# Kernel tuning notes

Measured on AMD Instinct MI355X. Metric: run time of the kernel, lower is better.

Reference implementation:

```python
import jax, jax.numpy as jnp
import numpy as np

B, T, D, H = 2, 2048, 1024, 16
Dh = D // H


def _rope(q, k):
    # q, k: (B, H, T, Dh), interleaved even/odd rotation
    t = q.shape[2]
    dh = q.shape[3]
    inv_freq = 1.0 / (10000.0 ** (jnp.arange(0, dh, 2, dtype=jnp.float32) / dh))
    pos = jnp.arange(t, dtype=jnp.float32)
    freqs = pos[:, None] * inv_freq[None, :]          # (T, Dh/2)
    sin = jnp.sin(freqs)[None, None]                  # (1,1,T,Dh/2)
    cos = jnp.cos(freqs)[None, None]

    def rot(x):
        xe, xo = x[..., ::2], x[..., 1::2]
        re = xe * cos - xo * sin
        ro = xe * sin + xo * cos
        return jnp.stack([re, ro], axis=-1).reshape(x.shape)

    return rot(q), rot(k)


def setup_inputs() -> dict:
    key = jax.random.key(0)
    k1, k2, k3 = jax.random.split(key, 3)
    s = 1.0 / np.sqrt(D)
    return {
        "x": jax.random.normal(k1, (B, T, D), dtype=jnp.float32),
        "w_qkv": jax.random.normal(k2, (3 * D, D), dtype=jnp.float32) * s,
        "b_qkv": jnp.zeros((3 * D,), dtype=jnp.float32),
        "w_out": jax.random.normal(k3, (D, D), dtype=jnp.float32) * s,
        "b_out": jnp.zeros((D,), dtype=jnp.float32),
    }


def reference(x, w_qkv, b_qkv, w_out, b_out):
    b, t, d = x.shape
    qkv = x @ w_qkv.T + b_qkv                         # (B,T,3D)
    q, k, v = jnp.split(qkv, 3, axis=-1)
    q = q.reshape(b, t, H, Dh).transpose(0, 2, 1, 3)  # (B,H,T,Dh)
    k = k.reshape(b, t, H, Dh).transpose(0, 2, 1, 3)
    v = v.reshape(b, t, H, Dh).transpose(0, 2, 1, 3)
    q, k = _rope(q, k)
    scores = jnp.einsum("bhtd,bhsd->bhts", q, k) / jnp.sqrt(jnp.float32(Dh))
    causal = jnp.tril(jnp.ones((t, t), dtype=bool))[None, None]
    scores = jnp.where(causal, scores, -jnp.inf)
    probs = jax.nn.softmax(scores, axis=-1)
    out = jnp.einsum("bhts,bhsd->bhtd", probs, v)     # (B,H,T,Dh)
    out = out.transpose(0, 2, 1, 3).reshape(b, t, d)
    return out @ w_out.T + b_out
```

## Files before the change

kernel.cpp:

```cpp
#include <hip/hip_runtime.h>
#include <hip/hip_bf16.h>
#include <math.h>
#include <type_traits>

#define B_ 2
#define T_ 2048
#define D_ 1024
#define H_ 16
#define DH_ 64

typedef __bf16 bf16_t;
typedef bf16_t bf16x8 __attribute__((ext_vector_type(8)));
typedef bf16_t bf16x4 __attribute__((ext_vector_type(4)));
typedef float f32x4 __attribute__((ext_vector_type(4)));

typedef __attribute__((address_space(1))) const void gas_void;
typedef __attribute__((address_space(3))) void las_void;

__device__ __forceinline__ void gld16(const void* g, void* l) {
    __builtin_amdgcn_global_load_lds((gas_void*)g, (las_void*)l, 16, 0, 0);
}

__global__ __launch_bounds__(256) void cvt3(const float* __restrict__ a,
                                            const float* __restrict__ b,
                                            const float* __restrict__ c,
                                            bf16_t* __restrict__ oa,
                                            bf16_t* __restrict__ ob,
                                            bf16_t* __restrict__ oc) {
    int i = blockIdx.x * 256 + threadIdx.x;
    const float* src; bf16_t* dst; int off;
    if (i < 1048576)      { src = a; dst = oa; off = i; }
    else if (i < 1835008) { src = b; dst = ob; off = i - 1048576; }
    else                  { src = c; dst = oc; off = i - 1835008; }
    float4 f = ((const float4*)src)[off];
    bf16x4 v = { (bf16_t)f.x, (bf16_t)f.y, (bf16_t)f.z, (bf16_t)f.w };
    ((bf16x4*)dst)[off] = v;
}

__global__ __launch_bounds__(256) void rope_tab_k(float2* __restrict__ tab) {
    int i = blockIdx.x * 256 + threadIdx.x;
    int t = i >> 5, d2 = i & 31;
    float invf = exp2f(-(float)d2 * 0.4152410118609203f);
    float ang = (float)t * invf;
    float sn, cs;
    sincosf(ang, &sn, &cs);
    tab[i] = make_float2(cs, sn);
}

template<int EPI>
__global__ __launch_bounds__(256) void gemm128(const bf16_t* __restrict__ A,
                                               const bf16_t* __restrict__ Bw,
                                               const float* __restrict__ bias,
                                               const float2* __restrict__ tab,
                                               bf16_t* __restrict__ q_out,
                                               bf16_t* __restrict__ k_out,
                                               bf16_t* __restrict__ vt_out,
                                               float* __restrict__ f_out,
                                               int K, int N) {
    __shared__ __align__(16) char smem[49152];
    char* b0 = smem;
    char* b1 = smem + 16384;
    char* b2 = smem + 32768;

    int tid = threadIdx.x;
    int lane = tid & 63, wid = tid >> 6;
    int wr = wid >> 1, wc = wid & 1;
    int lr = lane & 15, lk = lane >> 4;

    int l = blockIdx.y * gridDim.x + blockIdx.x;
    int chunk = (gridDim.x * gridDim.y) >> 3;
    int u = (l & 7) * chunk + (l >> 3);
    int bx = u % gridDim.x;
    int by = u / gridDim.x;

    f32x4 acc[4][4];
    f32x4 z = {0.f, 0.f, 0.f, 0.f};
#pragma unroll
    for (int i = 0; i < 4; i++)
#pragma unroll
        for (int j = 0; j < 4; j++) acc[i][j] = z;

    const char* Ab = (const char*)(A + (size_t)by * 128 * K);
    const char* Bb = (const char*)(Bw + (size_t)bx * 128 * K);
    const int rowstride = K * 2;

    int p0 = tid * 16;
    int p1 = 4096 + tid * 16;
    int r0 = p0 >> 6, r1 = p1 >> 6;
    int cb0 = (p0 & 63) ^ (((r0 >> 1) & 3) << 4);
    int cb1 = (p1 & 63) ^ (((r1 >> 1) & 3) << 4);
    size_t gA0 = (size_t)r0 * rowstride + cb0;
    size_t gA1 = (size_t)r1 * rowstride + cb1;

    int oa[4], ob[4];
#pragma unroll
    for (int m = 0; m < 4; m++) {
        int row = wr * 64 + m * 16 + lr;
        oa[m] = row * 64 + ((lk * 16) ^ (((row >> 1) & 3) << 4));
    }
#pragma unroll
    for (int n = 0; n < 4; n++) {
        int row = wc * 64 + n * 16 + lr;
        ob[n] = row * 64 + ((lk * 16) ^ (((row >> 1) & 3) << 4));
    }

    auto stg = [&](char* buf, int ks) __attribute__((always_inline)) {
        const char* Ag = Ab + (size_t)ks * 64;
        const char* Bg = Bb + (size_t)ks * 64;
        gld16(Ag + gA0, buf + p0);
        gld16(Ag + gA1, buf + p1);
        gld16(Bg + gA0, buf + 8192 + p0);
        gld16(Bg + gA1, buf + 8192 + p1);
    };

    auto iterf = [&](auto vmc, char* buf, int ks, bool dostage) __attribute__((always_inline)) {
        constexpr int VM = decltype(vmc)::value;
        if constexpr (VM == 8)      asm volatile("s_waitcnt vmcnt(8)" ::: "memory");
        else if constexpr (VM == 4) asm volatile("s_waitcnt vmcnt(4)" ::: "memory");
        else                        asm volatile("s_waitcnt vmcnt(0)" ::: "memory");
        __builtin_amdgcn_s_barrier();
        asm volatile("" ::: "memory");
        bf16x8 Af[4], Bf[4];
#pragma unroll
        for (int m = 0; m < 4; m++) Af[m] = *(const bf16x8*)(buf + oa[m]);
#pragma unroll
        for (int n = 0; n < 4; n++) Bf[n] = *(const bf16x8*)(buf + 8192 + ob[n]);
#pragma unroll
        for (int m = 0; m < 4; m++)
#pragma unroll
            for (int n = 0; n < 4; n++)
                acc[m][n] = __builtin_amdgcn_mfma_f32_16x16x32_bf16(Af[m], Bf[n], acc[m][n], 0, 0, 0);
        asm volatile("" ::: "memory");
        __builtin_amdgcn_s_barrier();
        asm volatile("" ::: "memory");
        if (dostage) stg(buf, ks);
    };

    std::integral_constant<int, 8> c8;
    std::integral_constant<int, 4> c4;
    std::integral_constant<int, 0> c0;

    stg(b0, 0);
    stg(b1, 1);
    stg(b2, 2);
    for (int s = 0; s < 30; s += 3) {
        iterf(c8, b0, s + 3, s + 3 < 32);
        iterf(c8, b1, s + 4, s + 4 < 32);
        iterf(c8, b2, s + 5, s + 5 < 32);
    }
    iterf(c4, b0, 0, false);
    iterf(c0, b1, 0, false);

    int m_base = by * 128 + wr * 64;
    int n_base = bx * 128 + wc * 64;
    if (EPI == 1) {
#pragma unroll
        for (int m = 0; m < 4; m++) {
            int gm0 = m_base + m * 16 + lk * 4;
#pragma unroll
            for (int n = 0; n < 4; n++) {
                int nc = n_base + n * 16 + lr;
                float bv = bias[nc];
#pragma unroll
                for (int j = 0; j < 4; j++)
                    f_out[(size_t)(gm0 + j) * N + nc] = acc[m][n][j] + bv;
            }
        }
    } else {
        char* myL = smem + wid * 8192;
        int which = n_base >> 10;
        int h = (n_base & 1023) >> 6;
        int b = m_base >> 11, t0 = m_base & 2047;
        int bh = b * H_ + h;
        if (which == 2) {
#pragma unroll
            for (int m = 0; m < 4; m++)
#pragma unroll
                for (int n = 0; n < 4; n++) {
                    int rd = n * 16 + lr;
                    float bv = bias[n_base + rd];
#pragma unroll
                    for (int j = 0; j < 4; j++) {
                        int ct = m * 16 + lk * 4 + j;
                        int ct2 = (ct & 32) | (((ct >> 2) & 3) << 3) | (((ct >> 4) & 1) << 2) | (ct & 3);
                        int addr = (rd * 128 + ct2 * 2) ^ ((rd & 7) << 4);
                        *(bf16_t*)(myL + addr) = (bf16_t)(acc[m][n][j] + bv);
                    }
                }
#pragma unroll
            for (int it = 0; it < 8; it++) {
                int row = it * 8 + (lane >> 3);
                int byte = (lane & 7) * 16;
                bf16x8 val = *(const bf16x8*)(myL + ((row * 128 + byte) ^ ((row & 7) << 4)));
                *(bf16x8*)(vt_out + ((size_t)bh * DH_ + row) * T_ + t0 + (lane & 7) * 8) = val;
            }
        } else {
            bf16_t* dst = which ? k_out : q_out;
            float qscl = which ? 1.0f : 0.18033688011112042f;
#pragma unroll
            for (int m = 0; m < 4; m++)
#pragma unroll
                for (int n = 0; n < 4; n++) {
                    int dh = n * 16 + lr;
                    float bv = bias[n_base + dh];
                    int dh2 = dh >> 1;
                    bool even = (dh & 1) == 0;
#pragma unroll
                    for (int j = 0; j < 4; j++) {
                        int rt = m * 16 + lk * 4 + j;
                        float v = acc[m][n][j] + bv;
                        float p = __shfl_xor(v, 1);
                        float2 cs = tab[(t0 + rt) * 32 + dh2];
                        float r = even ? v * cs.x - p * cs.y : v * cs.x + p * cs.y;
                        r *= qscl;
                        int addr = (rt * 128 + dh * 2) ^ ((rt & 7) << 4);
                        *(bf16_t*)(myL + addr) = (bf16_t)r;
                    }
                }
#pragma unroll
            for (int it = 0; it < 8; it++) {
                int row = it * 8 + (lane >> 3);
                int byte = (lane & 7) * 16;
                bf16x8 val = *(const bf16x8*)(myL + ((row * 128 + byte) ^ ((row & 7) << 4)));
                *(bf16x8*)(dst + ((size_t)bh * T_ + t0 + row) * DH_ + (lane & 7) * 8) = val;
            }
        }
    }
}

__global__ __launch_bounds__(256, 4) void attn64(const bf16_t* __restrict__ Q,
                                                 const bf16_t* __restrict__ K,
                                                 const bf16_t* __restrict__ Vt,
                                                 bf16_t* __restrict__ Ao) {
    __shared__ __align__(16) char smem[40960];

    int tid = threadIdx.x;
    int lane = tid & 63, wid = tid >> 6;
    int lr = lane & 15, lk = lane >> 4;
    int xcd = blockIdx.x & 7, idx = blockIdx.x >> 3;
    int bh = xcd * 4 + (idx & 3);
    int i5 = idx >> 2;
    int qq = i5 & 7, rr = i5 >> 3;
    int qt = (rr == 0) ? qq : (rr == 1) ? 15 - qq : (rr == 2) ? 16 + qq : 31 - qq;
    int q0 = qt * 64;
    int qrel = wid * 16 + lr;

    const bf16_t* Qp = Q + ((size_t)bh * T_ + q0 + qrel) * DH_;
    bf16x8 qf0 = *(const bf16x8*)(Qp + lk * 8);
    bf16x8 qf1 = *(const bf16x8*)(Qp + 32 + lk * 8);

    f32x4 zz = {0.f, 0.f, 0.f, 0.f};
    f32x4 oacc[4];
#pragma unroll
    for (int dt = 0; dt < 4; dt++) oacc[dt] = zz;
    float mrun = -__builtin_inff(), lsum = 0.f;

    const char* Kbase = (const char*)(K + (size_t)bh * T_ * DH_);
    const char* Vbase = (const char*)(Vt + (size_t)bh * DH_ * T_);

    auto stage = [&](int s, char* Kd, char* Vd) __attribute__((always_inline)) {
        int kv0 = s * 64;
        const char* Kg = Kbase + (size_t)kv0 * 128;
#pragma unroll
        for (int c = 0; c < 2; c++) {
            int o = c * 4096 + tid * 16;
            int r = o >> 7;
            int g = o ^ ((r & 7) << 4);
            gld16(Kg + g, Kd + o);
            gld16(Vbase + (size_t)r * (T_ * 2) + kv0 * 2 + (g & 127), Vd + o);
        }
    };

    float p[4][4];
    bf16x8 pb0, pb1;

    auto do_qk = [&](const char* Kc, auto dmc) __attribute__((always_inline)) {
        constexpr bool DM = decltype(dmc)::value;
#pragma unroll
        for (int kt = 0; kt < 4; kt++) {
            int row = kt * 16 + lr;
            int key = (row & 7) << 4;
            bf16x8 kf0 = *(const bf16x8*)(Kc + ((row * 128 + lk * 16) ^ key));
            bf16x8 kf1 = *(const bf16x8*)(Kc + ((row * 128 + 64 + lk * 16) ^ key));
            f32x4 sacc = zz;
            sacc = __builtin_amdgcn_mfma_f32_16x16x32_bf16(kf0, qf0, sacc, 0, 0, 0);
            sacc = __builtin_amdgcn_mfma_f32_16x16x32_bf16(kf1, qf1, sacc, 0, 0, 0);
#pragma unroll
            for (int j = 0; j < 4; j++) {
                if (DM) {
                    int kvrel = kt * 16 + lk * 4 + j;
                    p[kt][j] = (kvrel <= qrel) ? sacc[j] : -__builtin_inff();
                } else {
                    p[kt][j] = sacc[j];
                }
            }
        }
    };

    auto do_pv = [&](const char* Vc) __attribute__((always_inline)) {
#pragma unroll
        for (int dt = 0; dt < 4; dt++) {
            int row = dt * 16 + lr;
            int key = (row & 7) << 4;
            bf16x8 vf0 = *(const bf16x8*)(Vc + ((row * 128 + lk * 16) ^ key));
            bf16x8 vf1 = *(const bf16x8*)(Vc + ((row * 128 + 64 + lk * 16) ^ key));
            f32x4 o = oacc[dt];
            o = __builtin_amdgcn_mfma_f32_16x16x32_bf16(vf0, pb0, o, 0, 0, 0);
            o = __builtin_amdgcn_mfma_f32_16x16x32_bf16(vf1, pb1, o, 0, 0, 0);
            oacc[dt] = o;
        }
    };

    auto do_softmax = [&]() __attribute__((always_inline)) {
        float mk[4];
#pragma unroll
        for (int kt = 0; kt < 4; kt++)
            mk[kt] = fmaxf(fmaxf(p[kt][0], p[kt][1]), fmaxf(p[kt][2], p[kt][3]));
        float mx = fmaxf(fmaxf(mk[0], mk[1]), fmaxf(mk[2], mk[3]));
        mx = fmaxf(mx, __shfl_xor(mx, 16));
        mx = fmaxf(mx, __shfl_xor(mx, 32));
        if (!__all(mx <= mrun + 8.f)) {
            float mnew = fmaxf(mrun, mx);
            float fac = exp2f(mrun - mnew);
            mrun = mnew;
            lsum *= fac;
#pragma unroll
            for (int dt = 0; dt < 4; dt++) oacc[dt] = oacc[dt] * fac;
        }
        float rs = 0.f;
#pragma unroll
        for (int kt = 0; kt < 4; kt++)
#pragma unroll
            for (int j = 0; j < 4; j++) {
                float e = exp2f(p[kt][j] - mrun);
                p[kt][j] = e;
                rs += e;
            }
        rs += __shfl_xor(rs, 16);
        rs += __shfl_xor(rs, 32);
        lsum += rs;
        pb0 = bf16x8{ (bf16_t)p[0][0], (bf16_t)p[0][1], (bf16_t)p[0][2], (bf16_t)p[0][3],
                      (bf16_t)p[1][0], (bf16_t)p[1][1], (bf16_t)p[1][2], (bf16_t)p[1][3] };
        pb1 = bf16x8{ (bf16_t)p[2][0], (bf16_t)p[2][1], (bf16_t)p[2][2], (bf16_t)p[2][3],
                      (bf16_t)p[3][0], (bf16_t)p[3][1], (bf16_t)p[3][2], (bf16_t)p[3][3] };
    };

    std::integral_constant<bool, true>  mask_y;
    std::integral_constant<bool, false> mask_n;

    stage(0, smem, smem + 16384);
    stage(1, smem + 8192, smem + 24576);
    asm volatile("s_waitcnt vmcnt(4)" ::: "memory");
    __builtin_amdgcn_s_barrier();
    asm volatile("" ::: "memory");
    if (qt == 0) do_qk(smem, mask_y); else do_qk(smem, mask_n);
    do_softmax();

    char* Kr = smem + 8192;
    char* Kw = smem;
    char* Vr = smem + 16384;
    char* Vn = smem + 24576;
    char* Vw = smem + 32768;

    auto iter = [&](int s, auto dmc) __attribute__((always_inline)) {
        asm volatile("s_waitcnt vmcnt(0)" ::: "memory");
        __builtin_amdgcn_s_barrier();
        asm volatile("" ::: "memory");
        if (s + 2 <= qt) stage(s + 2, Kw, Vw);
        do_qk(Kr, dmc);
        do_pv(Vr);
        do_softmax();
        char* t;
        t = Kr; Kr = Kw; Kw = t;
        t = Vr; Vr = Vn; Vn = Vw; Vw = t;
    };

    for (int s = 0; s + 1 < qt; ++s) iter(s, mask_n);
    if (qt > 0) iter(qt - 1, mask_y);
    do_pv(Vr);
    __syncthreads();

    char* myL = smem + wid * 2048;
    float rinv = __builtin_amdgcn_rcpf(lsum);
#pragma unroll
    for (int dt = 0; dt < 4; dt++)
#pragma unroll
        for (int j = 0; j < 4; j++) {
            int dh = dt * 16 + lk * 4 + j;
            int addr = (lr * 128 + dh * 2) ^ ((lr & 7) << 4);
            *(bf16_t*)(myL + addr) = (bf16_t)(oacc[dt][j] * rinv);
        }
    int b = bh >> 4, h = bh & 15;
#pragma unroll
    for (int it = 0; it < 2; it++) {
        int row = it * 8 + (lane >> 3);
        int byte = (lane & 7) * 16;
        bf16x8 val = *(const bf16x8*)(myL + ((row * 128 + byte) ^ ((row & 7) << 4)));
        int t = q0 + wid * 16 + row;
        *(bf16x8*)(Ao + ((size_t)b * T_ + t) * D_ + h * DH_ + (lane & 7) * 8) = val;
    }
}

extern "C" void kernel_launch(void* const* d_in, const int* in_sizes, int n_in,
                              void* d_out, int out_size, void* d_ws, size_t ws_size,
                              hipStream_t stream) {
    const float* x     = (const float*)d_in[0];
    const float* w_qkv = (const float*)d_in[1];
    const float* b_qkv = (const float*)d_in[2];
    const float* w_out = (const float*)d_in[3];
    const float* b_out = (const float*)d_in[4];
    float* out = (float*)d_out;

    char* ws = (char*)d_ws;
    bf16_t* xb    = (bf16_t*)(ws);
    bf16_t* wqkvb = (bf16_t*)(ws + 8388608);
    bf16_t* wob   = (bf16_t*)(ws + 14680064);
    bf16_t* qb    = (bf16_t*)(ws + 16777216);
    bf16_t* kb    = (bf16_t*)(ws + 25165824);
    bf16_t* vtb   = (bf16_t*)(ws + 33554432);
    bf16_t* ab    = (bf16_t*)(ws + 41943040);
    float2* tab   = (float2*)(ws + 41943040);

    rope_tab_k<<<256, 256, 0, stream>>>(tab);
    cvt3<<<8192, 256, 0, stream>>>(x, w_qkv, w_out, xb, wqkvb, wob);

    gemm128<0><<<dim3(24, 32), 256, 0, stream>>>(xb, wqkvb, b_qkv, tab, qb, kb, vtb, nullptr, 1024, 3072);
    attn64<<<1024, 256, 0, stream>>>(qb, kb, vtb, ab);
    gemm128<1><<<dim3(8, 32), 256, 0, stream>>>(ab, wob, b_out, nullptr, nullptr, nullptr, nullptr, out, 1024, 1024);
}
```

Measured before the change: 115.9 us.

## Replace QKV projection with 256x256-tile 8-wave GEMM using double-buffered LDS

The QKV projection moves from a 128x128-tile, 4-wave kernel to a dedicated 256x256-tile, 8-wave kernel with 128KB of double-buffered LDS. Global-to-LDS loads for the next k-step are interleaved with MFMA phases, separated by explicit barriers and s_setprio. The larger tile raises arithmetic intensity and halves operand re-reads from L2, and the grid is remapped to spread blocks across XCDs. The cost is one block per CU (192 blocks for 256 CUs, so some CUs sit idle) and many barriers per k-step. The output GEMM is split into its own non-templated kernel with the same behaviour.

```diff
diff --git a/kernel.cpp b/kernel.cpp
--- a/kernel.cpp
+++ b/kernel.cpp
@@ -20,6 +20,8 @@
 __device__ __forceinline__ void gld16(const void* g, void* l) {
     __builtin_amdgcn_global_load_lds((gas_void*)g, (las_void*)l, 16, 0, 0);
 }
+
+#define BARRIER() do { asm volatile("" ::: "memory"); __builtin_amdgcn_s_barrier(); asm volatile("" ::: "memory"); } while (0)
 
 __global__ __launch_bounds__(256) void cvt3(const float* __restrict__ a,
                                             const float* __restrict__ b,
@@ -47,16 +49,181 @@
     tab[i] = make_float2(cs, sn);
 }
 
-template<int EPI>
-__global__ __launch_bounds__(256) void gemm128(const bf16_t* __restrict__ A,
-                                               const bf16_t* __restrict__ Bw,
-                                               const float* __restrict__ bias,
-                                               const float2* __restrict__ tab,
-                                               bf16_t* __restrict__ q_out,
-                                               bf16_t* __restrict__ k_out,
-                                               bf16_t* __restrict__ vt_out,
-                                               float* __restrict__ f_out,
-                                               int K, int N) {
+__global__ __launch_bounds__(512, 1) void gemm256qkv(const bf16_t* __restrict__ A,
+                                                     const bf16_t* __restrict__ Bw,
+                                                     const float* __restrict__ bias,
+                                                     const float2* __restrict__ tab,
+                                                     bf16_t* __restrict__ q_out,
+                                                     bf16_t* __restrict__ k_out,
+                                                     bf16_t* __restrict__ vt_out) {
+    __shared__ __align__(16) char smem[131072];
+
+    int tid = threadIdx.x;
+    int lane = tid & 63, wid = tid >> 6;
+    int wm = wid >> 2, wn = wid & 3;
+    int lr = lane & 15, lk = lane >> 4;
+
+    int l = blockIdx.y * 12 + blockIdx.x;
+    int x = l & 7, c = l >> 3;
+    int by = x * 2 + (c >= 12);
+    int bx = (c >= 12) ? c - 12 : c;
+
+    f32x4 acc[8][4];
+    f32x4 z = {0.f, 0.f, 0.f, 0.f};
+#pragma unroll
+    for (int i = 0; i < 8; i++)
+#pragma unroll
+        for (int j = 0; j < 4; j++) acc[i][j] = z;
+
+    int colb = (tid * 16) & 127;
+    int rb = tid >> 3;
+    int csw = colb ^ ((rb & 7) << 4);
+    const char* gA = (const char*)A + (size_t)(by * 256 + rb) * 2048 + csw;
+    const char* gB = (const char*)Bw + (size_t)(bx * 256 + rb) * 2048 + csw;
+
+    auto stgA = [&](int par, int h, int kt) __attribute__((always_inline)) {
+        char* d = smem + par * 32768 + h * 16384;
+        const char* g = gA + (size_t)h * 262144 + kt * 128;
+        gld16(g, d + tid * 16);
+        gld16(g + 131072, d + 8192 + tid * 16);
+    };
+    auto stgB = [&](int par, int h, int kt) __attribute__((always_inline)) {
+        char* d = smem + 65536 + par * 32768 + h * 16384;
+        const char* g = gB + (size_t)h * 262144 + kt * 128;
+        gld16(g, d + tid * 16);
+        gld16(g + 131072, d + 8192 + tid * 16);
+    };
+
+    int swz = (lr & 7) << 4;
+    int ca0 = (lk * 16) ^ swz;
+    int ca1 = (64 + lk * 16) ^ swz;
+
+    bf16x8 Af[2][2], Bf[4][2];
+    auto rdB = [&](const char* cB) __attribute__((always_inline)) {
+        const char* base = cB + (wn >> 1) * 16384 + ((wn & 1) * 64) * 128 + lr * 128;
+#pragma unroll
+        for (int n = 0; n < 4; n++) {
+            Bf[n][0] = *(const bf16x8*)(base + n * 2048 + ca0);
+            Bf[n][1] = *(const bf16x8*)(base + n * 2048 + ca1);
+        }
+    };
+    auto rdA = [&](const char* cA, int mp) __attribute__((always_inline)) {
+        const char* base = cA + wm * 16384 + lr * 128;
+#pragma unroll
+        for (int mm = 0; mm < 2; mm++) {
+            Af[mm][0] = *(const bf16x8*)(base + (mp * 2 + mm) * 2048 + ca0);
+            Af[mm][1] = *(const bf16x8*)(base + (mp * 2 + mm) * 2048 + ca1);
+        }
+    };
+    auto mfmaset = [&](int q) __attribute__((always_inline)) {
+        __builtin_amdgcn_s_setprio(1);
+#pragma unroll
+        for (int mm = 0; mm < 2; mm++)
+#pragma unroll
+            for (int n = 0; n < 4; n++)
+#pragma unroll
+                for (int ks = 0; ks < 2; ks++)
+                    acc[q * 2 + mm][n] = __builtin_amdgcn_mfma_f32_16x16x32_bf16(
+                        Af[mm][ks], Bf[n][ks], acc[q * 2 + mm][n], 0, 0, 0);
+        __builtin_amdgcn_s_setprio(0);
+    };
+
+    stgA(0, 0, 0); stgA(0, 1, 0); stgB(0, 0, 0); stgB(0, 1, 0);
+
+    for (int kt = 0; kt < 15; ++kt) {
+        int p = kt & 1, np = p ^ 1;
+        const char* cA = smem + p * 32768;
+        const char* cB = smem + 65536 + p * 32768;
+        stgA(np, 0, kt + 1);
+        asm volatile("s_waitcnt vmcnt(2)" ::: "memory");
+        BARRIER();
+        rdB(cB); rdA(cA, 0); stgA(np, 1, kt + 1);
+        BARRIER(); mfmaset(0); BARRIER();
+        rdA(cA, 1); stgB(np, 0, kt + 1);
+        BARRIER(); mfmaset(1); BARRIER();
+        rdA(cA, 2); stgB(np, 1, kt + 1);
+        BARRIER(); mfmaset(2); BARRIER();
+        rdA(cA, 3);
+        BARRIER(); mfmaset(3); BARRIER();
+    }
+    {
+        const char* cA = smem + 32768;
+        const char* cB = smem + 65536 + 32768;
+        asm volatile("s_waitcnt vmcnt(0)" ::: "memory");
+        BARRIER();
+        rdB(cB); rdA(cA, 0); BARRIER(); mfmaset(0); BARRIER();
+        rdA(cA, 1); BARRIER(); mfmaset(1); BARRIER();
+        rdA(cA, 2); BARRIER(); mfmaset(2); BARRIER();
+        rdA(cA, 3); BARRIER(); mfmaset(3); BARRIER();
+    }
+
+    int m_base = by * 256 + wm * 128;
+    int n_base = bx * 256 + wn * 64;
+    char* myL = smem + wid * 16384;
+    int which = n_base >> 10;
+    int h = (n_base & 1023) >> 6;
+    int b = m_base >> 11, t0 = m_base & 2047;
+    int bh = b * H_ + h;
+    if (which == 2) {
+#pragma unroll
+        for (int m = 0; m < 8; m++)
+#pragma unroll
+            for (int n = 0; n < 4; n++) {
+                int rd = n * 16 + lr;
+                float bv = bias[n_base + rd];
+#pragma unroll
+                for (int j = 0; j < 4; j++) {
+                    int ct = m * 16 + lk * 4 + j;
+                    int ct2 = (ct & 96) | (((ct >> 2) & 3) << 3) | (((ct >> 4) & 1) << 2) | (ct & 3);
+                    int addr = (rd * 256 + ct2 * 2) ^ ((rd & 7) << 4);
+                    *(bf16_t*)(myL + addr) = (bf16_t)(acc[m][n][j] + bv);
+                }
+            }
+#pragma unroll
+        for (int it = 0; it < 16; it++) {
+            int row = it * 4 + (lane >> 4);
+            int byt = (lane & 15) * 16;
+            bf16x8 val = *(const bf16x8*)(myL + ((row * 256 + byt) ^ ((row & 7) << 4)));
+            *(bf16x8*)(vt_out + ((size_t)bh * DH_ + row) * T_ + t0 + (lane & 15) * 8) = val;
+        }
+    } else {
+        bf16_t* dst = which ? k_out : q_out;
+        float qscl = which ? 1.0f : 0.18033688011112042f;
+#pragma unroll
+        for (int m = 0; m < 8; m++)
+#pragma unroll
+            for (int n = 0; n < 4; n++) {
+                int dh = n * 16 + lr;
+                float bv = bias[n_base + dh];
+                int dh2 = dh >> 1;
+                bool even = (dh & 1) == 0;
+#pragma unroll
+                for (int j = 0; j < 4; j++) {
+                    int rt = m * 16 + lk * 4 + j;
+                    float v = acc[m][n][j] + bv;
+                    float pp = __shfl_xor(v, 1);
+                    float2 cs = tab[(t0 + rt) * 32 + dh2];
+                    float r = even ? v * cs.x - pp * cs.y : v * cs.x + pp * cs.y;
+                    r *= qscl;
+                    int addr = (rt * 128 + dh * 2) ^ ((rt & 7) << 4);
+                    *(bf16_t*)(myL + addr) = (bf16_t)r;
+                }
+            }
+#pragma unroll
+        for (int it = 0; it < 16; it++) {
+            int row = it * 8 + (lane >> 3);
+            int byt = (lane & 7) * 16;
+            bf16x8 val = *(const bf16x8*)(myL + ((row * 128 + byt) ^ ((row & 7) << 4)));
+            *(bf16x8*)(dst + ((size_t)bh * T_ + t0 + row) * DH_ + (lane & 7) * 8) = val;
+        }
+    }
+}
+
+__global__ __launch_bounds__(256) void gemm128o(const bf16_t* __restrict__ A,
+                                                const bf16_t* __restrict__ Bw,
+                                                const float* __restrict__ bias,
+                                                float* __restrict__ f_out,
+                                                int K, int N) {
     __shared__ __align__(16) char smem[49152];
     char* b0 = smem;
     char* b1 = smem + 16384;
@@ -153,77 +320,16 @@
 
     int m_base = by * 128 + wr * 64;
     int n_base = bx * 128 + wc * 64;
-    if (EPI == 1) {
-#pragma unroll
-        for (int m = 0; m < 4; m++) {
-            int gm0 = m_base + m * 16 + lk * 4;
-#pragma unroll
-            for (int n = 0; n < 4; n++) {
-                int nc = n_base + n * 16 + lr;
-                float bv = bias[nc];
-#pragma unroll
-                for (int j = 0; j < 4; j++)
-                    f_out[(size_t)(gm0 + j) * N + nc] = acc[m][n][j] + bv;
-            }
-        }
-    } else {
-        char* myL = smem + wid * 8192;
-        int which = n_base >> 10;
-        int h = (n_base & 1023) >> 6;
-        int b = m_base >> 11, t0 = m_base & 2047;
-        int bh = b * H_ + h;
-        if (which == 2) {
-#pragma unroll
-            for (int m = 0; m < 4; m++)
-#pragma unroll
-                for (int n = 0; n < 4; n++) {
-                    int rd = n * 16 + lr;
-                    float bv = bias[n_base + rd];
-#pragma unroll
-                    for (int j = 0; j < 4; j++) {
-                        int ct = m * 16 + lk * 4 + j;
-                        int ct2 = (ct & 32) | (((ct >> 2) & 3) << 3) | (((ct >> 4) & 1) << 2) | (ct & 3);
-                        int addr = (rd * 128 + ct2 * 2) ^ ((rd & 7) << 4);
-                        *(bf16_t*)(myL + addr) = (bf16_t)(acc[m][n][j] + bv);
-                    }
-                }
-#pragma unroll
-            for (int it = 0; it < 8; it++) {
-                int row = it * 8 + (lane >> 3);
-                int byte = (lane & 7) * 16;
-                bf16x8 val = *(const bf16x8*)(myL + ((row * 128 + byte) ^ ((row & 7) << 4)));
-                *(bf16x8*)(vt_out + ((size_t)bh * DH_ + row) * T_ + t0 + (lane & 7) * 8) = val;
-            }
-        } else {
-            bf16_t* dst = which ? k_out : q_out;
-            float qscl = which ? 1.0f : 0.18033688011112042f;
-#pragma unroll
-            for (int m = 0; m < 4; m++)
-#pragma unroll
-                for (int n = 0; n < 4; n++) {
-                    int dh = n * 16 + lr;
-                    float bv = bias[n_base + dh];
-                    int dh2 = dh >> 1;
-                    bool even = (dh & 1) == 0;
-#pragma unroll
-                    for (int j = 0; j < 4; j++) {
-                        int rt = m * 16 + lk * 4 + j;
-                        float v = acc[m][n][j] + bv;
-                        float p = __shfl_xor(v, 1);
-                        float2 cs = tab[(t0 + rt) * 32 + dh2];
-                        float r = even ? v * cs.x - p * cs.y : v * cs.x + p * cs.y;
-                        r *= qscl;
-                        int addr = (rt * 128 + dh * 2) ^ ((rt & 7) << 4);
-                        *(bf16_t*)(myL + addr) = (bf16_t)r;
-                    }
-                }
-#pragma unroll
-            for (int it = 0; it < 8; it++) {
-                int row = it * 8 + (lane >> 3);
-                int byte = (lane & 7) * 16;
-                bf16x8 val = *(const bf16x8*)(myL + ((row * 128 + byte) ^ ((row & 7) << 4)));
-                *(bf16x8*)(dst + ((size_t)bh * T_ + t0 + row) * DH_ + (lane & 7) * 8) = val;
-            }
+#pragma unroll
+    for (int m = 0; m < 4; m++) {
+        int gm0 = m_base + m * 16 + lk * 4;
+#pragma unroll
+        for (int n = 0; n < 4; n++) {
+            int nc = n_base + n * 16 + lr;
+            float bv = bias[nc];
+#pragma unroll
+            for (int j = 0; j < 4; j++)
+                f_out[(size_t)(gm0 + j) * N + nc] = acc[m][n][j] + bv;
         }
     }
 }
@@ -394,8 +500,8 @@
 #pragma unroll
     for (int it = 0; it < 2; it++) {
         int row = it * 8 + (lane >> 3);
-        int byte = (lane & 7) * 16;
-        bf16x8 val = *(const bf16x8*)(myL + ((row * 128 + byte) ^ ((row & 7) << 4)));
+        int byt = (lane & 7) * 16;
+        bf16x8 val = *(const bf16x8*)(myL + ((row * 128 + byt) ^ ((row & 7) << 4)));
         int t = q0 + wid * 16 + row;
         *(bf16x8*)(Ao + ((size_t)b * T_ + t) * D_ + h * DH_ + (lane & 7) * 8) = val;
     }
@@ -424,7 +530,7 @@
     rope_tab_k<<<256, 256, 0, stream>>>(tab);
     cvt3<<<8192, 256, 0, stream>>>(x, w_qkv, w_out, xb, wqkvb, wob);
 
-    gemm128<0><<<dim3(24, 32), 256, 0, stream>>>(xb, wqkvb, b_qkv, tab, qb, kb, vtb, nullptr, 1024, 3072);
+    gemm256qkv<<<dim3(12, 16), 512, 0, stream>>>(xb, wqkvb, b_qkv, tab, qb, kb, vtb);
     attn64<<<1024, 256, 0, stream>>>(qb, kb, vtb, ab);
-    gemm128<1><<<dim3(8, 32), 256, 0, stream>>>(ab, wob, b_out, nullptr, nullptr, nullptr, nullptr, out, 1024, 1024);
-}
+    gemm128o<<<dim3(8, 32), 256, 0, stream>>>(ab, wob, b_out, out, 1024, 1024);
+}
```

Result: no change. 114.5 us (-1.2%).
